# Kernel tuning notes

Hardware: AMD Instinct MI355X
Metric: run time of the kernel (lower is better)

## Reference

```python
import jax, jax.numpy as jnp
import numpy as np

NUM_EXPERTS = 8
TOP_K = 2
EMBED = 1024
FFN = 2048
GATE_HID = 1024


def setup_inputs() -> dict:
    key = jax.random.key(0)
    ks = jax.random.split(key, 8)
    s_e = 1.0 / np.sqrt(EMBED)
    s_f = 1.0 / np.sqrt(FFN)
    s_g = 1.0 / np.sqrt(GATE_HID)
    return {
        "hidden_states": jax.random.normal(ks[0], (2, 2048, EMBED), dtype=jnp.float32),
        # gate: Linear(EMBED->GATE_HID) with bias, ELU, Linear(GATE_HID->NUM_EXPERTS) with bias
        "gw1": jax.random.uniform(ks[1], (EMBED, GATE_HID), jnp.float32, -s_e, s_e),
        "gb1": jax.random.uniform(ks[2], (GATE_HID,), jnp.float32, -s_e, s_e),
        "gw2": jax.random.uniform(ks[3], (GATE_HID, NUM_EXPERTS), jnp.float32, -s_g, s_g),
        "gb2": jax.random.uniform(ks[4], (NUM_EXPERTS,), jnp.float32, -s_g, s_g),
        # experts (bias=False): w1,w3: EMBED->FFN ; w2: FFN->EMBED, stacked over experts
        "w1": jax.random.uniform(ks[5], (NUM_EXPERTS, EMBED, FFN), jnp.float32, -s_e, s_e),
        "w3": jax.random.uniform(ks[6], (NUM_EXPERTS, EMBED, FFN), jnp.float32, -s_e, s_e),
        "w2": jax.random.uniform(ks[7], (NUM_EXPERTS, FFN, EMBED), jnp.float32, -s_f, s_f),
    }


def reference(hidden_states, gw1, gb1, gw2, gb2, w1, w3, w2):
    B, S, H = hidden_states.shape
    x = hidden_states.reshape(-1, H)                      # [T, H]
    T = x.shape[0]
    # gate MLP
    g = jax.nn.elu(x @ gw1 + gb1)
    router_logits = g @ gw2 + gb2                         # [T, E]
    probs = jax.nn.softmax(router_logits.astype(jnp.float32), axis=-1)
    rw, sel = jax.lax.top_k(probs, TOP_K)                 # [T, K]
    rw = rw / jnp.sum(rw, axis=-1, keepdims=True)
    rw = rw.astype(hidden_states.dtype)
    # combine weights per (token, expert); full-capacity MoE == weighted sum
    combine = jnp.zeros((T, NUM_EXPERTS), dtype=hidden_states.dtype)
    combine = combine.at[jnp.arange(T)[:, None], sel].add(rw)   # [T, E]
    # expert MLPs computed densely then combined (math identical to gather/scatter)
    h = jax.nn.relu(jnp.einsum('th,ehf->etf', x, w1)) * jnp.einsum('th,ehf->etf', x, w3)
    y = jnp.einsum('etf,efh->eth', h, w2)                 # [E, T, H]
    out = jnp.einsum('eth,te->th', y, combine)            # [T, H]
    return out.reshape(B, S, H), router_logits
```

## Files before the change

kernel.cpp:

```cpp
#include <hip/hip_runtime.h>
#include <hip/hip_bf16.h>
#include <stdint.h>

#define TOKENS 4096
#define HDIM   1024
#define FDIM   2048
#define NEXP   8
#define NSLOTS (2 * TOKENS)
#define SLOTPAD (NSLOTS + 128)
#define RISKY_CAP 256
#define FLAG_THR 6e-3f

typedef __attribute__((ext_vector_type(4))) float        f32x4v;
typedef __attribute__((ext_vector_type(2))) float        f32x2v;
typedef __attribute__((ext_vector_type(4))) unsigned int u32x4v;
typedef __attribute__((ext_vector_type(8))) _Float16     f16x8v;

__device__ __forceinline__ unsigned short f2h(float f) {
  _Float16 h = (_Float16)f;
  union { _Float16 h; unsigned short u; } x; x.h = h; return x.u;
}

__device__ __forceinline__ void gload16(void* lds, const void* g) {
  __builtin_amdgcn_global_load_lds(
      reinterpret_cast<const __attribute__((address_space(1))) uint32_t*>(
          reinterpret_cast<uintptr_t>(g)),
      reinterpret_cast<__attribute__((address_space(3))) uint32_t*>(
          reinterpret_cast<uintptr_t>(lds)),
      16, 0, 0);
}

__global__ void k_convert_xh(const float* __restrict__ in, unsigned short* __restrict__ out) {
  const int i = (blockIdx.x * 256 + threadIdx.x) * 8;
  f32x4v a = *(const f32x4v*)(in + i);
  f32x4v b = *(const f32x4v*)(in + i + 4);
  u32x4v r;
  r[0] = (uint32_t)f2h(a[0]) | ((uint32_t)f2h(a[1]) << 16);
  r[1] = (uint32_t)f2h(a[2]) | ((uint32_t)f2h(a[3]) << 16);
  r[2] = (uint32_t)f2h(b[0]) | ((uint32_t)f2h(b[1]) << 16);
  r[3] = (uint32_t)f2h(b[2]) | ((uint32_t)f2h(b[3]) << 16);
  *(u32x4v*)(out + i) = r;
}

__device__ __forceinline__ void transpose_tile_v2(const float* __restrict__ ip,
                                                  unsigned short* __restrict__ op,
                                                  int R, int C, int r0, int c0) {
  __shared__ unsigned short tile[64][70];
  const int t = threadIdx.x;
  const int cp = (t & 15) * 4;
  const int rp = (t >> 4) * 2;
#pragma unroll
  for (int p = 0; p < 2; ++p) {
    const int r = rp + p * 32;
    f32x4v v0 = *(const f32x4v*)(ip + (size_t)(r0 + r) * C + c0 + cp);
    f32x4v v1 = *(const f32x4v*)(ip + (size_t)(r0 + r + 1) * C + c0 + cp);
#pragma unroll
    for (int j = 0; j < 4; ++j)
      *(uint32_t*)&tile[cp + j][r] = (uint32_t)f2h(v0[j]) | ((uint32_t)f2h(v1[j]) << 16);
  }
  __syncthreads();
  const int c = t >> 2, rc = (t & 3) * 16;
  uint32_t q[8];
#pragma unroll
  for (int j = 0; j < 8; ++j) q[j] = *(uint32_t*)&tile[c][rc + j * 2];
  unsigned short* o = op + (size_t)(c0 + c) * R + r0 + rc;
  u32x4v s0, s1;
  s0[0] = q[0]; s0[1] = q[1]; s0[2] = q[2]; s0[3] = q[3];
  s1[0] = q[4]; s1[1] = q[5]; s1[2] = q[6]; s1[3] = q[7];
  *(u32x4v*)o = s0;
  *(u32x4v*)(o + 8) = s1;
}

__global__ __launch_bounds__(256)
void k_transpose_v2(const float* __restrict__ in, unsigned short* __restrict__ out,
                    int R, int C) {
  const size_t mat = (size_t)R * C;
  transpose_tile_v2(in + (size_t)blockIdx.z * mat, out + (size_t)blockIdx.z * mat,
                    R, C, blockIdx.y * 64, blockIdx.x * 64);
}

__global__ __launch_bounds__(256)
void k_transpose_w13_v2(const float* __restrict__ w1, const float* __restrict__ w3,
                        unsigned short* __restrict__ o1, unsigned short* __restrict__ o3) {
  const int R = 1024, C = 2048;
  const size_t mat = (size_t)R * C;
  const int e = blockIdx.z & 7, which = blockIdx.z >> 3;
  const float* ip = (which ? w3 : w1) + (size_t)e * mat;
  unsigned short* op = (which ? o3 : o1) + (size_t)e * mat;
  transpose_tile_v2(ip, op, R, C, blockIdx.y * 64, blockIdx.x * 64);
}

__global__ __launch_bounds__(256)
void k_gate_f16(const unsigned short* __restrict__ Xh, const unsigned short* __restrict__ Bt,
                const float* __restrict__ gb1, float* __restrict__ G) {
  const int n0 = blockIdx.x * 64, m0 = blockIdx.y * 128;
  __shared__ unsigned short lA[128 * 64];
  __shared__ unsigned short lB[64 * 64];
  const int t = threadIdx.x, lane = t & 63, wv = t >> 6;

  const unsigned short *ap[4], *bp[2];
#pragma unroll
  for (int i = 0; i < 4; ++i) {
    const int gi = wv * 4 + i;
    const int row = gi * 8 + (lane >> 3);
    const int cs = (lane & 7) ^ (row & 7);
    ap[i] = Xh + (size_t)(m0 + row) * HDIM + cs * 8;
  }
#pragma unroll
  for (int i = 0; i < 2; ++i) {
    const int gi = wv * 2 + i;
    const int row = gi * 8 + (lane >> 3);
    const int cs = (lane & 7) ^ (row & 7);
    bp[i] = Bt + (size_t)(n0 + row) * HDIM + cs * 8;
  }

  f32x4v acc[4][2];
#pragma unroll
  for (int m = 0; m < 4; ++m)
#pragma unroll
    for (int n = 0; n < 2; ++n) acc[m][n] = (f32x4v){0.f, 0.f, 0.f, 0.f};

  const int wr = (wv >> 1) * 64, wc = (wv & 1) * 32;

  for (int k0 = 0; k0 < HDIM; k0 += 64) {
#pragma unroll
    for (int i = 0; i < 4; ++i) gload16(lA + (wv * 4 + i) * 512, ap[i] + k0);
#pragma unroll
    for (int i = 0; i < 2; ++i) gload16(lB + (wv * 2 + i) * 512, bp[i] + k0);
    __syncthreads();
#pragma unroll
    for (int kk = 0; kk < 2; ++kk) {
      const int ch = kk * 4 + (lane >> 4);
      f16x8v af[4];
#pragma unroll
      for (int m = 0; m < 4; ++m) {
        const int r = wr + m * 16 + (lane & 15);
        af[m] = *(const f16x8v*)(lA + r * 64 + (ch ^ (r & 7)) * 8);
      }
#pragma unroll
      for (int n = 0; n < 2; ++n) {
        const int r = wc + n * 16 + (lane & 15);
        f16x8v b = *(const f16x8v*)(lB + r * 64 + (ch ^ (r & 7)) * 8);
#pragma unroll
        for (int m = 0; m < 4; ++m)
          acc[m][n] = __builtin_amdgcn_mfma_f32_16x16x32_f16(af[m], b, acc[m][n], 0, 0, 0);
      }
    }
    __syncthreads();
  }
#pragma unroll
  for (int m = 0; m < 4; ++m)
#pragma unroll
    for (int n = 0; n < 2; ++n)
#pragma unroll
      for (int q = 0; q < 4; ++q) {
        const int row = m0 + wr + m * 16 + ((lane >> 4) << 2) + q;
        const int col = n0 + wc + n * 16 + (lane & 15);
        float x = acc[m][n][q] + gb1[col];
        G[(size_t)row * 1024 + col] = x > 0.f ? x : expm1f(x);
      }
}

__global__ void k_logits(const float* __restrict__ G, const float* __restrict__ gw2,
                         const float* __restrict__ gb2, float* __restrict__ Lg,
                         int* __restrict__ risky, int* __restrict__ rcnt) {
  const int lane = threadIdx.x & 63, wv = threadIdx.x >> 6;
  const int tok = blockIdx.x * 4 + wv;
  const float* g = G + (size_t)tok * 1024 + lane * 16;
  float acc[8];
#pragma unroll
  for (int j = 0; j < 8; ++j) acc[j] = 0.f;
#pragma unroll
  for (int c = 0; c < 16; c += 4) {
    f32x4v gv = *(const f32x4v*)(g + c);
#pragma unroll
    for (int u = 0; u < 4; ++u) {
      const float* wrow = gw2 + (size_t)(lane * 16 + c + u) * 8;
      f32x4v w0 = *(const f32x4v*)wrow;
      f32x4v w1 = *(const f32x4v*)(wrow + 4);
#pragma unroll
      for (int j = 0; j < 4; ++j) {
        acc[j]     += gv[u] * w0[j];
        acc[j + 4] += gv[u] * w1[j];
      }
    }
  }
#pragma unroll
  for (int s = 1; s < 64; s <<= 1)
#pragma unroll
    for (int j = 0; j < 8; ++j) acc[j] += __shfl_xor(acc[j], s, 64);
  if (lane == 0) {
    float l[8];
#pragma unroll
    for (int j = 0; j < 8; ++j) { l[j] = acc[j] + gb2[j]; Lg[(size_t)tok * 8 + j] = l[j]; }
    int i0 = 0; float v0 = l[0];
#pragma unroll
    for (int j = 1; j < 8; ++j) if (l[j] > v0) { v0 = l[j]; i0 = j; }
    int i1 = (i0 == 0) ? 1 : 0; float v1 = l[i1];
#pragma unroll
    for (int j = 0; j < 8; ++j) if (j != i0 && l[j] > v1) { v1 = l[j]; i1 = j; }
    float v2 = -1e30f;
#pragma unroll
    for (int j = 0; j < 8; ++j) if (j != i0 && j != i1 && l[j] > v2) v2 = l[j];
    if (v1 - v2 < FLAG_THR) {
      const int pos = atomicAdd(rcnt, 1);
      if (pos < RISKY_CAP) risky[pos] = tok;
    }
  }
}

__global__ __launch_bounds__(256)
void k_fixup_gs(const float* __restrict__ X, const float* __restrict__ gw1,
                const float* __restrict__ gb1, const int* __restrict__ risky,
                const int* __restrict__ rcnt, float* __restrict__ gsbuf) {
  __shared__ float xs[1024];
  __shared__ float red[128];
  int n = *rcnt; if (n > RISKY_CAP) n = RISKY_CAP;
  const int idx = blockIdx.y;
  if (idx >= n) return;
  const int tok = risky[idx];
  const int s0 = blockIdx.x * 128;
  const int t = threadIdx.x;
  for (int i = t; i < 1024; i += 256) xs[i] = X[(size_t)tok * 1024 + i];
  __syncthreads();
  const int h = t & 127, kh = t >> 7;
  const float* wp = gw1 + (size_t)(kh * 512) * 1024 + s0 + h;
  const float* xp = xs + kh * 512;
  float a0 = 0.f, a1 = 0.f, a2 = 0.f, a3 = 0.f;
  for (int k = 0; k < 512; k += 4) {
    a0 += xp[k]     * wp[(size_t)k * 1024];
    a1 += xp[k + 1] * wp[(size_t)(k + 1) * 1024];
    a2 += xp[k + 2] * wp[(size_t)(k + 2) * 1024];
    a3 += xp[k + 3] * wp[(size_t)(k + 3) * 1024];
  }
  const float acc = (a0 + a1) + (a2 + a3);
  if (kh == 1) red[h] = acc;
  __syncthreads();
  if (kh == 0) {
    const float v = acc + red[h] + gb1[s0 + h];
    gsbuf[(size_t)idx * 1024 + s0 + h] = v > 0.f ? v : expm1f(v);
  }
}

__global__ __launch_bounds__(256)
void k_fixup_lg(const float* __restrict__ gsbuf, const float* __restrict__ gw2,
                const float* __restrict__ gb2, const int* __restrict__ risky,
                const int* __restrict__ rcnt, float* __restrict__ Lg) {
  __shared__ float part[4][8];
  int n = *rcnt; if (n > RISKY_CAP) n = RISKY_CAP;
  const int idx = blockIdx.x;
  if (idx >= n) return;
  const int tok = risky[idx];
  const int t = threadIdx.x, lane = t & 63, wv = t >> 6;
  float lacc[8];
#pragma unroll
  for (int e = 0; e < 8; ++e) lacc[e] = 0.f;
#pragma unroll
  for (int j = 0; j < 4; ++j) {
    const int k = t * 4 + j;
    const float gv = gsbuf[(size_t)idx * 1024 + k];
    const float* w = gw2 + (size_t)k * 8;
#pragma unroll
    for (int e = 0; e < 8; ++e) lacc[e] += gv * w[e];
  }
#pragma unroll
  for (int s = 1; s < 64; s <<= 1)
#pragma unroll
    for (int e = 0; e < 8; ++e) lacc[e] += __shfl_xor(lacc[e], s, 64);
  if (lane == 0) {
#pragma unroll
    for (int e = 0; e < 8; ++e) part[wv][e] = lacc[e];
  }
  __syncthreads();
  if (t < 8) Lg[(size_t)tok * 8 + t] = part[0][t] + part[1][t] + part[2][t] + part[3][t] + gb2[t];
}

__global__ void k_top2(const float* __restrict__ Lg, int* __restrict__ tok_e,
                       float* __restrict__ tok_w, int* __restrict__ counts) {
  const int t = blockIdx.x * 256 + threadIdx.x;
  float l[8];
#pragma unroll
  for (int j = 0; j < 8; ++j) l[j] = Lg[(size_t)t * 8 + j];
  float mx = l[0];
#pragma unroll
  for (int j = 1; j < 8; ++j) mx = fmaxf(mx, l[j]);
  float p[8];
#pragma unroll
  for (int j = 0; j < 8; ++j) p[j] = expf(l[j] - mx);
  int i0 = 0; float b0 = p[0];
#pragma unroll
  for (int j = 1; j < 8; ++j) if (p[j] > b0) { b0 = p[j]; i0 = j; }
  int i1 = (i0 == 0) ? 1 : 0; float b1 = p[i1];
#pragma unroll
  for (int j = 0; j < 8; ++j) if (j != i0 && p[j] > b1) { b1 = p[j]; i1 = j; }
  const float inv = 1.f / (b0 + b1);
  tok_e[2 * t] = i0; tok_e[2 * t + 1] = i1;
  tok_w[2 * t] = b0 * inv; tok_w[2 * t + 1] = b1 * inv;
  atomicAdd(&counts[i0], 1);
  atomicAdd(&counts[i1], 1);
}

__global__ void k_offsets(const int* __restrict__ counts, int* __restrict__ offs,
                          int* __restrict__ curs) {
  if (threadIdx.x == 0) {
    int a = 0;
#pragma unroll
    for (int e = 0; e < NEXP; ++e) { offs[e] = a; a += counts[e]; }
  }
  if (threadIdx.x < NEXP) curs[threadIdx.x] = 0;
}

__global__ void k_assign(const int* __restrict__ tok_e, const float* __restrict__ tok_w,
                         const int* __restrict__ offs, int* __restrict__ curs,
                         int* __restrict__ slot_tok, float* __restrict__ slot_w,
                         int* __restrict__ tok2slot) {
  const int t = blockIdx.x * 256 + threadIdx.x;
#pragma unroll
  for (int k = 0; k < 2; ++k) {
    const int e = tok_e[2 * t + k];
    const int pos = atomicAdd(&curs[e], 1);
    const int slot = offs[e] + pos;
    slot_tok[slot] = t;
    slot_w[slot] = tok_w[2 * t + k];
    tok2slot[2 * t + k] = slot;
  }
}

__global__ __launch_bounds__(256, 2)
void k_gemm1(const unsigned short* __restrict__ Xh, const unsigned short* __restrict__ w1T,
             const unsigned short* __restrict__ w3T, const int* __restrict__ slot_tok,
             const int* __restrict__ counts, const int* __restrict__ offs,
             unsigned short* __restrict__ Hout) {
  const int e = blockIdx.z;
  const int cnt = counts[e];
  const int mt = blockIdx.y;
  if (mt * 128 >= cnt) return;
  const int base = offs[e] + mt * 128;
  const int n0 = blockIdx.x * 128;

  __shared__ unsigned short lA[128 * 64];
  __shared__ unsigned short lB1[128 * 64];
  __shared__ unsigned short lB3[128 * 64];
  __shared__ int tokid[128];

  const int t = threadIdx.x;
  if (t < 128) tokid[t] = slot_tok[base + t];
  __syncthreads();

  const int lane = t & 63, wv = t >> 6;
  const unsigned short *arow[4], *b1row[4], *b3row[4];
#pragma unroll
  for (int i = 0; i < 4; ++i) {
    const int gi = wv * 4 + i;
    const int row = gi * 8 + (lane >> 3);
    const int cs = (lane & 7) ^ (row & 7);
    arow[i] = Xh + (size_t)tokid[row] * HDIM + cs * 8;
    const int f = n0 + row;
    b1row[i] = w1T + ((size_t)e * FDIM + f) * HDIM + cs * 8;
    b3row[i] = w3T + ((size_t)e * FDIM + f) * HDIM + cs * 8;
  }

  f32x4v acc1[4][4], acc3[4][4];
#pragma unroll
  for (int m = 0; m < 4; ++m)
#pragma unroll
    for (int n = 0; n < 4; ++n) {
      acc1[m][n] = (f32x4v){0.f, 0.f, 0.f, 0.f};
      acc3[m][n] = (f32x4v){0.f, 0.f, 0.f, 0.f};
    }
  const int wr = (wv >> 1) * 64, wc = (wv & 1) * 64;

  for (int k0 = 0; k0 < HDIM; k0 += 64) {
#pragma unroll
    for (int i = 0; i < 4; ++i) {
      gload16(lA + (wv * 4 + i) * 512, arow[i] + k0);
      gload16(lB1 + (wv * 4 + i) * 512, b1row[i] + k0);
      gload16(lB3 + (wv * 4 + i) * 512, b3row[i] + k0);
    }
    __syncthreads();
#pragma unroll
    for (int kk = 0; kk < 64; kk += 32) {
      const int ch = (kk >> 3) + (lane >> 4);
      f16x8v af[4];
#pragma unroll
      for (int m = 0; m < 4; ++m) {
        const int r = wr + m * 16 + (lane & 15);
        af[m] = *(const f16x8v*)(lA + r * 64 + (ch ^ (r & 7)) * 8);
      }
#pragma unroll
      for (int n = 0; n < 4; ++n) {
        const int r = wc + n * 16 + (lane & 15);
        const int o = r * 64 + (ch ^ (r & 7)) * 8;
        f16x8v b1 = *(const f16x8v*)(lB1 + o);
        f16x8v b3 = *(const f16x8v*)(lB3 + o);
#pragma unroll
        for (int m = 0; m < 4; ++m) {
          acc1[m][n] = __builtin_amdgcn_mfma_f32_16x16x32_f16(af[m], b1, acc1[m][n], 0, 0, 0);
          acc3[m][n] = __builtin_amdgcn_mfma_f32_16x16x32_f16(af[m], b3, acc3[m][n], 0, 0, 0);
        }
      }
    }
    __syncthreads();
  }

  const int maxr = cnt - mt * 128;
#pragma unroll
  for (int m = 0; m < 4; ++m)
#pragma unroll
    for (int q = 0; q < 4; ++q) {
      const int rl = wr + m * 16 + ((lane >> 4) << 2) + q;
      if (rl < maxr) {
        unsigned short* hrow = Hout + (size_t)(base + rl) * FDIM;
#pragma unroll
        for (int n = 0; n < 4; ++n) {
          const int col = n0 + wc + n * 16 + (lane & 15);
          const float h = fmaxf(acc1[m][n][q], 0.f) * acc3[m][n][q];
          hrow[col] = f2h(h);
        }
      }
    }
}

__global__ __launch_bounds__(256, 2)
void k_gemm2(const unsigned short* __restrict__ Hin, const unsigned short* __restrict__ w2T,
             const int* __restrict__ counts, const int* __restrict__ offs,
             unsigned short* __restrict__ Y) {
  const int e = blockIdx.z;
  const int cnt = counts[e];
  const int mt = blockIdx.y;
  if (mt * 128 >= cnt) return;
  const int base = offs[e] + mt * 128;
  const int n0 = blockIdx.x * 128;

  __shared__ unsigned short lA[128 * 64];
  __shared__ unsigned short lB[128 * 64];

  const int t = threadIdx.x, lane = t & 63, wv = t >> 6;
  const unsigned short *arow[4], *brow[4];
#pragma unroll
  for (int i = 0; i < 4; ++i) {
    const int gi = wv * 4 + i;
    const int row = gi * 8 + (lane >> 3);
    const int cs = (lane & 7) ^ (row & 7);
    arow[i] = Hin + (size_t)(base + row) * FDIM + cs * 8;
    brow[i] = w2T + ((size_t)e * HDIM + n0 + row) * FDIM + cs * 8;
  }

  f32x4v acc[4][4];
#pragma unroll
  for (int m = 0; m < 4; ++m)
#pragma unroll
    for (int n = 0; n < 4; ++n) acc[m][n] = (f32x4v){0.f, 0.f, 0.f, 0.f};

  const int wr = (wv >> 1) * 64, wc = (wv & 1) * 64;

  for (int k0 = 0; k0 < FDIM; k0 += 64) {
#pragma unroll
    for (int i = 0; i < 4; ++i) {
      gload16(lA + (wv * 4 + i) * 512, arow[i] + k0);
      gload16(lB + (wv * 4 + i) * 512, brow[i] + k0);
    }
    __syncthreads();
#pragma unroll
    for (int kk = 0; kk < 64; kk += 32) {
      const int ch = (kk >> 3) + (lane >> 4);
      f16x8v af[4];
#pragma unroll
      for (int m = 0; m < 4; ++m) {
        const int r = wr + m * 16 + (lane & 15);
        af[m] = *(const f16x8v*)(lA + r * 64 + (ch ^ (r & 7)) * 8);
      }
#pragma unroll
      for (int n = 0; n < 4; ++n) {
        const int r = wc + n * 16 + (lane & 15);
        f16x8v b = *(const f16x8v*)(lB + r * 64 + (ch ^ (r & 7)) * 8);
#pragma unroll
        for (int m = 0; m < 4; ++m)
          acc[m][n] = __builtin_amdgcn_mfma_f32_16x16x32_f16(af[m], b, acc[m][n], 0, 0, 0);
      }
    }
    __syncthreads();
  }

  const int maxr = cnt - mt * 128;
#pragma unroll
  for (int m = 0; m < 4; ++m)
#pragma unroll
    for (int q = 0; q < 4; ++q) {
      const int rl = wr + m * 16 + ((lane >> 4) << 2) + q;
      if (rl < maxr) {
        unsigned short* yrow = Y + (size_t)(base + rl) * HDIM;
#pragma unroll
        for (int n = 0; n < 4; ++n) {
          const int col = n0 + wc + n * 16 + (lane & 15);
          yrow[col] = f2h(acc[m][n][q]);
        }
      }
    }
}

__global__ __launch_bounds__(256)
void k_combine(const unsigned short* __restrict__ Y, const int* __restrict__ tok2slot,
               const float* __restrict__ slot_w, float* __restrict__ out) {
  const int tok = blockIdx.x;
  const int s0 = tok2slot[2 * tok], s1 = tok2slot[2 * tok + 1];
  const float w0 = slot_w[s0], w1 = slot_w[s1];
  const int i = threadIdx.x * 4;
  const _Float16* y0 = (const _Float16*)(Y + (size_t)s0 * HDIM + i);
  const _Float16* y1 = (const _Float16*)(Y + (size_t)s1 * HDIM + i);
  f32x4v r;
#pragma unroll
  for (int j = 0; j < 4; ++j) r[j] = w0 * (float)y0[j] + w1 * (float)y1[j];
  *(f32x4v*)(out + (size_t)tok * HDIM + i) = r;
}

extern "C" void kernel_launch(void* const* d_in, const int* in_sizes, int n_in,
                              void* d_out, int out_size, void* d_ws, size_t ws_size,
                              hipStream_t stream) {
  const float* X   = (const float*)d_in[0];
  const float* gw1 = (const float*)d_in[1];
  const float* gb1 = (const float*)d_in[2];
  const float* gw2 = (const float*)d_in[3];
  const float* gb2 = (const float*)d_in[4];
  const float* w1  = (const float*)d_in[5];
  const float* w3  = (const float*)d_in[6];
  const float* w2  = (const float*)d_in[7];

  float* out = (float*)d_out;
  float* Lg  = out + (size_t)TOKENS * HDIM;

  char* ws = (char*)d_ws;
  size_t off = 0;
  auto alloc = [&](size_t b) { void* p = ws + off; off = (off + b + 255) & ~(size_t)255; return p; };

  unsigned short* Xh    = (unsigned short*)alloc((size_t)TOKENS * HDIM * 2);
  unsigned short* gw1T  = (unsigned short*)alloc((size_t)HDIM * 1024 * 2);
  unsigned short* w1T   = (unsigned short*)alloc((size_t)NEXP * FDIM * HDIM * 2);
  unsigned short* w3T   = (unsigned short*)alloc((size_t)NEXP * FDIM * HDIM * 2);
  unsigned short* w2T   = (unsigned short*)alloc((size_t)NEXP * HDIM * FDIM * 2);
  float*          G     = (float*)alloc((size_t)TOKENS * 1024 * 4);
  unsigned short* Hf    = (unsigned short*)alloc((size_t)SLOTPAD * FDIM * 2);
  unsigned short* Yb    = (unsigned short*)alloc((size_t)SLOTPAD * HDIM * 2);
  float*          gsbuf = (float*)alloc((size_t)RISKY_CAP * 1024 * 4);
  int*   tok_e    = (int*)alloc((size_t)TOKENS * 2 * 4);
  float* tok_w    = (float*)alloc((size_t)TOKENS * 2 * 4);
  int*   tok2slot = (int*)alloc((size_t)TOKENS * 2 * 4);
  int*   counts   = (int*)alloc(64);
  int*   offs     = (int*)alloc(64);
  int*   curs     = (int*)alloc(64);
  int*   slot_tok = (int*)alloc((size_t)SLOTPAD * 4);
  float* slot_w   = (float*)alloc((size_t)SLOTPAD * 4);
  int*   risky    = (int*)alloc((size_t)RISKY_CAP * 4);
  int*   rcnt     = (int*)alloc(64);

  hipMemsetAsync(counts, 0, 64, stream);
  hipMemsetAsync(rcnt, 0, 64, stream);
  hipMemsetAsync(slot_tok, 0, (size_t)SLOTPAD * 4, stream);

  k_convert_xh<<<dim3(TOKENS * HDIM / 2048), 256, 0, stream>>>(X, Xh);
  k_transpose_w13_v2<<<dim3(FDIM / 64, HDIM / 64, 2 * NEXP), 256, 0, stream>>>(w1, w3, w1T, w3T);
  k_transpose_v2<<<dim3(HDIM / 64, FDIM / 64, NEXP), 256, 0, stream>>>(w2, w2T, FDIM, HDIM);
  k_transpose_v2<<<dim3(16, 16, 1), 256, 0, stream>>>(gw1, gw1T, 1024, 1024);
  k_gate_f16<<<dim3(1024 / 64, TOKENS / 128), 256, 0, stream>>>(Xh, gw1T, gb1, G);
  k_logits<<<dim3(TOKENS / 4), 256, 0, stream>>>(G, gw2, gb2, Lg, risky, rcnt);
  k_fixup_gs<<<dim3(8, RISKY_CAP), 256, 0, stream>>>(X, gw1, gb1, risky, rcnt, gsbuf);
  k_fixup_lg<<<dim3(RISKY_CAP), 256, 0, stream>>>(gsbuf, gw2, gb2, risky, rcnt, Lg);
  k_top2<<<dim3(TOKENS / 256), 256, 0, stream>>>(Lg, tok_e, tok_w, counts);
  k_offsets<<<dim3(1), 64, 0, stream>>>(counts, offs, curs);
  k_assign<<<dim3(TOKENS / 256), 256, 0, stream>>>(tok_e, tok_w, offs, curs, slot_tok, slot_w, tok2slot);
  k_gemm1<<<dim3(FDIM / 128, TOKENS / 128, NEXP), 256, 0, stream>>>(Xh, w1T, w3T, slot_tok, counts, offs, Hf);
  k_gemm2<<<dim3(HDIM / 128, TOKENS / 128, NEXP), 256, 0, stream>>>(Hf, w2T, counts, offs, Yb);
  k_combine<<<dim3(TOKENS), 256, 0, stream>>>(Yb, tok2slot, slot_w, out);
}
```

Baseline: 373.5 us.

## Fuse gate GEMM, X conversion and weight transposes into one launch

Merges the X fp16 conversion, the w1/w3/w2 transposes and the gate GEMM into a single kernel that dispatches on block index, so the independent prep work can overlap with the gate GEMM. The gate GEMM now converts X from fp32 to fp16 on the fly instead of waiting for Xh. The gate hidden activations are stored as fp16 instead of fp32, which halves that traffic but adds rounding before the logits, which the risky-token fixup path must absorb. SLOTPAD is also enlarged.

```diff
diff --git a/kernel.cpp b/kernel.cpp
--- a/kernel.cpp
+++ b/kernel.cpp
@@ -7,12 +7,11 @@
 #define FDIM   2048
 #define NEXP   8
 #define NSLOTS (2 * TOKENS)
-#define SLOTPAD (NSLOTS + 128)
+#define SLOTPAD (NSLOTS + 256)
 #define RISKY_CAP 256
 #define FLAG_THR 6e-3f
 
 typedef __attribute__((ext_vector_type(4))) float        f32x4v;
-typedef __attribute__((ext_vector_type(2))) float        f32x2v;
 typedef __attribute__((ext_vector_type(4))) unsigned int u32x4v;
 typedef __attribute__((ext_vector_type(8))) _Float16     f16x8v;
 
@@ -30,18 +29,6 @@
       16, 0, 0);
 }
 
-__global__ void k_convert_xh(const float* __restrict__ in, unsigned short* __restrict__ out) {
-  const int i = (blockIdx.x * 256 + threadIdx.x) * 8;
-  f32x4v a = *(const f32x4v*)(in + i);
-  f32x4v b = *(const f32x4v*)(in + i + 4);
-  u32x4v r;
-  r[0] = (uint32_t)f2h(a[0]) | ((uint32_t)f2h(a[1]) << 16);
-  r[1] = (uint32_t)f2h(a[2]) | ((uint32_t)f2h(a[3]) << 16);
-  r[2] = (uint32_t)f2h(b[0]) | ((uint32_t)f2h(b[1]) << 16);
-  r[3] = (uint32_t)f2h(b[2]) | ((uint32_t)f2h(b[3]) << 16);
-  *(u32x4v*)(out + i) = r;
-}
-
 __device__ __forceinline__ void transpose_tile_v2(const float* __restrict__ ip,
                                                   unsigned short* __restrict__ op,
                                                   int R, int C, int r0, int c0) {
@@ -72,117 +59,152 @@
 }
 
 __global__ __launch_bounds__(256)
-void k_transpose_v2(const float* __restrict__ in, unsigned short* __restrict__ out,
-                    int R, int C) {
-  const size_t mat = (size_t)R * C;
-  transpose_tile_v2(in + (size_t)blockIdx.z * mat, out + (size_t)blockIdx.z * mat,
-                    R, C, blockIdx.y * 64, blockIdx.x * 64);
-}
-
+void k_prep0(const float* __restrict__ gw1, unsigned short* __restrict__ og1) {
+  transpose_tile_v2(gw1, og1, 1024, 1024, (blockIdx.x >> 4) * 64, (blockIdx.x & 15) * 64);
+}
+
+#define NB_GATE 512
+#define NB_CONV 2048
+#define NB_W13  8192
+#define NB_W2   4096
 __global__ __launch_bounds__(256)
-void k_transpose_w13_v2(const float* __restrict__ w1, const float* __restrict__ w3,
-                        unsigned short* __restrict__ o1, unsigned short* __restrict__ o3) {
-  const int R = 1024, C = 2048;
-  const size_t mat = (size_t)R * C;
-  const int e = blockIdx.z & 7, which = blockIdx.z >> 3;
-  const float* ip = (which ? w3 : w1) + (size_t)e * mat;
-  unsigned short* op = (which ? o3 : o1) + (size_t)e * mat;
-  transpose_tile_v2(ip, op, R, C, blockIdx.y * 64, blockIdx.x * 64);
-}
-
-__global__ __launch_bounds__(256)
-void k_gate_f16(const unsigned short* __restrict__ Xh, const unsigned short* __restrict__ Bt,
-                const float* __restrict__ gb1, float* __restrict__ G) {
-  const int n0 = blockIdx.x * 64, m0 = blockIdx.y * 128;
-  __shared__ unsigned short lA[128 * 64];
-  __shared__ unsigned short lB[64 * 64];
-  const int t = threadIdx.x, lane = t & 63, wv = t >> 6;
-
-  const unsigned short *ap[4], *bp[2];
-#pragma unroll
-  for (int i = 0; i < 4; ++i) {
-    const int gi = wv * 4 + i;
-    const int row = gi * 8 + (lane >> 3);
-    const int cs = (lane & 7) ^ (row & 7);
-    ap[i] = Xh + (size_t)(m0 + row) * HDIM + cs * 8;
-  }
-#pragma unroll
-  for (int i = 0; i < 2; ++i) {
-    const int gi = wv * 2 + i;
-    const int row = gi * 8 + (lane >> 3);
-    const int cs = (lane & 7) ^ (row & 7);
-    bp[i] = Bt + (size_t)(n0 + row) * HDIM + cs * 8;
-  }
-
-  f32x4v acc[4][2];
-#pragma unroll
-  for (int m = 0; m < 4; ++m)
-#pragma unroll
-    for (int n = 0; n < 2; ++n) acc[m][n] = (f32x4v){0.f, 0.f, 0.f, 0.f};
-
-  const int wr = (wv >> 1) * 64, wc = (wv & 1) * 32;
-
-  for (int k0 = 0; k0 < HDIM; k0 += 64) {
-#pragma unroll
-    for (int i = 0; i < 4; ++i) gload16(lA + (wv * 4 + i) * 512, ap[i] + k0);
-#pragma unroll
-    for (int i = 0; i < 2; ++i) gload16(lB + (wv * 2 + i) * 512, bp[i] + k0);
-    __syncthreads();
-#pragma unroll
-    for (int kk = 0; kk < 2; ++kk) {
-      const int ch = kk * 4 + (lane >> 4);
-      f16x8v af[4];
-#pragma unroll
-      for (int m = 0; m < 4; ++m) {
-        const int r = wr + m * 16 + (lane & 15);
-        af[m] = *(const f16x8v*)(lA + r * 64 + (ch ^ (r & 7)) * 8);
-      }
-#pragma unroll
-      for (int n = 0; n < 2; ++n) {
-        const int r = wc + n * 16 + (lane & 15);
-        f16x8v b = *(const f16x8v*)(lB + r * 64 + (ch ^ (r & 7)) * 8);
-#pragma unroll
-        for (int m = 0; m < 4; ++m)
-          acc[m][n] = __builtin_amdgcn_mfma_f32_16x16x32_f16(af[m], b, acc[m][n], 0, 0, 0);
-      }
-    }
-    __syncthreads();
-  }
-#pragma unroll
-  for (int m = 0; m < 4; ++m)
-#pragma unroll
-    for (int n = 0; n < 2; ++n)
-#pragma unroll
-      for (int q = 0; q < 4; ++q) {
-        const int row = m0 + wr + m * 16 + ((lane >> 4) << 2) + q;
-        const int col = n0 + wc + n * 16 + (lane & 15);
-        float x = acc[m][n][q] + gb1[col];
-        G[(size_t)row * 1024 + col] = x > 0.f ? x : expm1f(x);
-      }
-}
-
-__global__ void k_logits(const float* __restrict__ G, const float* __restrict__ gw2,
+void k_fused(const float* __restrict__ X, unsigned short* __restrict__ Xh,
+             const float* __restrict__ w1, const float* __restrict__ w3,
+             unsigned short* __restrict__ o1, unsigned short* __restrict__ o3,
+             const float* __restrict__ w2, unsigned short* __restrict__ o2,
+             const unsigned short* __restrict__ gw1T, const float* __restrict__ gb1,
+             unsigned short* __restrict__ Gh) {
+  const int id = blockIdx.x;
+  const int t = threadIdx.x;
+  if (id < NB_GATE) {
+    __shared__ unsigned short lA[128 * 64];
+    __shared__ unsigned short lB[64 * 64];
+    const int n0 = (id & 15) * 64, m0 = (id >> 4) * 128;
+    const int lane = t & 63, wv = t >> 6;
+
+    const unsigned short* bp[2];
+#pragma unroll
+    for (int i = 0; i < 2; ++i) {
+      const int gi = wv * 2 + i;
+      const int row = gi * 8 + (lane >> 3);
+      const int cs = (lane & 7) ^ (row & 7);
+      bp[i] = gw1T + (size_t)(n0 + row) * HDIM + cs * 8;
+    }
+
+    f32x4v acc[4][2];
+#pragma unroll
+    for (int m = 0; m < 4; ++m)
+#pragma unroll
+      for (int n = 0; n < 2; ++n) acc[m][n] = (f32x4v){0.f, 0.f, 0.f, 0.f};
+
+    const int wr = (wv >> 1) * 64, wc = (wv & 1) * 32;
+
+    for (int k0 = 0; k0 < HDIM; k0 += 64) {
+#pragma unroll
+      for (int p = 0; p < 4; ++p) {
+        const int ga = p * 256 + t;
+        const int r = ga >> 3, c = ga & 7;
+        const float* s = X + (size_t)(m0 + r) * HDIM + k0 + c * 8;
+        f32x4v v0 = *(const f32x4v*)s;
+        f32x4v v1 = *(const f32x4v*)(s + 4);
+        u32x4v pk;
+        pk[0] = (uint32_t)f2h(v0[0]) | ((uint32_t)f2h(v0[1]) << 16);
+        pk[1] = (uint32_t)f2h(v0[2]) | ((uint32_t)f2h(v0[3]) << 16);
+        pk[2] = (uint32_t)f2h(v1[0]) | ((uint32_t)f2h(v1[1]) << 16);
+        pk[3] = (uint32_t)f2h(v1[2]) | ((uint32_t)f2h(v1[3]) << 16);
+        *(u32x4v*)&lA[r * 64 + ((c ^ (r & 7)) * 8)] = pk;
+      }
+#pragma unroll
+      for (int i = 0; i < 2; ++i) gload16(lB + (wv * 2 + i) * 512, bp[i] + k0);
+      __syncthreads();
+#pragma unroll
+      for (int kk = 0; kk < 2; ++kk) {
+        const int ch = kk * 4 + (lane >> 4);
+        f16x8v af[4];
+#pragma unroll
+        for (int m = 0; m < 4; ++m) {
+          const int r = wr + m * 16 + (lane & 15);
+          af[m] = *(const f16x8v*)(lA + r * 64 + (ch ^ (r & 7)) * 8);
+        }
+#pragma unroll
+        for (int n = 0; n < 2; ++n) {
+          const int r = wc + n * 16 + (lane & 15);
+          f16x8v b = *(const f16x8v*)(lB + r * 64 + (ch ^ (r & 7)) * 8);
+#pragma unroll
+          for (int m = 0; m < 4; ++m)
+            acc[m][n] = __builtin_amdgcn_mfma_f32_16x16x32_f16(af[m], b, acc[m][n], 0, 0, 0);
+        }
+      }
+      __syncthreads();
+    }
+#pragma unroll
+    for (int m = 0; m < 4; ++m)
+#pragma unroll
+      for (int n = 0; n < 2; ++n)
+#pragma unroll
+        for (int q = 0; q < 4; ++q) {
+          const int row = m0 + wr + m * 16 + ((lane >> 4) << 2) + q;
+          const int col = n0 + wc + n * 16 + (lane & 15);
+          float x = acc[m][n][q] + gb1[col];
+          Gh[(size_t)row * 1024 + col] = f2h(x > 0.f ? x : expm1f(x));
+        }
+    return;
+  }
+  int b = id - NB_GATE;
+  if (b < NB_CONV) {
+    const int i = (b * 256 + t) * 8;
+    f32x4v a = *(const f32x4v*)(X + i);
+    f32x4v c = *(const f32x4v*)(X + i + 4);
+    u32x4v r;
+    r[0] = (uint32_t)f2h(a[0]) | ((uint32_t)f2h(a[1]) << 16);
+    r[1] = (uint32_t)f2h(a[2]) | ((uint32_t)f2h(a[3]) << 16);
+    r[2] = (uint32_t)f2h(c[0]) | ((uint32_t)f2h(c[1]) << 16);
+    r[3] = (uint32_t)f2h(c[2]) | ((uint32_t)f2h(c[3]) << 16);
+    *(u32x4v*)(Xh + i) = r;
+    return;
+  }
+  b -= NB_CONV;
+  if (b < NB_W13) {
+    const int bx = b & 31, by = (b >> 5) & 15, bz = b >> 9;
+    const int e = bz & 7, which = bz >> 3;
+    const size_t mat = (size_t)1024 * 2048;
+    transpose_tile_v2((which ? w3 : w1) + (size_t)e * mat,
+                      (which ? o3 : o1) + (size_t)e * mat,
+                      1024, 2048, by * 64, bx * 64);
+    return;
+  }
+  b -= NB_W13;
+  {
+    const int bx = b & 15, by = (b >> 4) & 31, e = b >> 9;
+    const size_t mat = (size_t)2048 * 1024;
+    transpose_tile_v2(w2 + (size_t)e * mat, o2 + (size_t)e * mat,
+                      2048, 1024, by * 64, bx * 64);
+  }
+}
+
+__global__ void k_logits(const unsigned short* __restrict__ Gh, const float* __restrict__ gw2,
                          const float* __restrict__ gb2, float* __restrict__ Lg,
                          int* __restrict__ risky, int* __restrict__ rcnt) {
   const int lane = threadIdx.x & 63, wv = threadIdx.x >> 6;
   const int tok = blockIdx.x * 4 + wv;
-  const float* g = G + (size_t)tok * 1024 + lane * 16;
+  const unsigned short* g = Gh + (size_t)tok * 1024 + lane * 16;
+  f16x8v g0 = *(const f16x8v*)g;
+  f16x8v g1 = *(const f16x8v*)(g + 8);
+  float gv[16];
+#pragma unroll
+  for (int j = 0; j < 8; ++j) { gv[j] = (float)g0[j]; gv[8 + j] = (float)g1[j]; }
   float acc[8];
 #pragma unroll
   for (int j = 0; j < 8; ++j) acc[j] = 0.f;
 #pragma unroll
-  for (int c = 0; c < 16; c += 4) {
-    f32x4v gv = *(const f32x4v*)(g + c);
-#pragma unroll
-    for (int u = 0; u < 4; ++u) {
-      const float* wrow = gw2 + (size_t)(lane * 16 + c + u) * 8;
-      f32x4v w0 = *(const f32x4v*)wrow;
-      f32x4v w1 = *(const f32x4v*)(wrow + 4);
-#pragma unroll
-      for (int j = 0; j < 4; ++j) {
-        acc[j]     += gv[u] * w0[j];
-        acc[j + 4] += gv[u] * w1[j];
-      }
+  for (int u = 0; u < 16; ++u) {
+    const float* wrow = gw2 + (size_t)(lane * 16 + u) * 8;
+    f32x4v w0 = *(const f32x4v*)wrow;
+    f32x4v w1 = *(const f32x4v*)(wrow + 4);
+#pragma unroll
+    for (int j = 0; j < 4; ++j) {
+      acc[j]     += gv[u] * w0[j];
+      acc[j + 4] += gv[u] * w1[j];
     }
   }
 #pragma unroll
@@ -538,7 +560,7 @@
   unsigned short* w1T   = (unsigned short*)alloc((size_t)NEXP * FDIM * HDIM * 2);
   unsigned short* w3T   = (unsigned short*)alloc((size_t)NEXP * FDIM * HDIM * 2);
   unsigned short* w2T   = (unsigned short*)alloc((size_t)NEXP * HDIM * FDIM * 2);
-  float*          G     = (float*)alloc((size_t)TOKENS * 1024 * 4);
+  unsigned short* Gh    = (unsigned short*)alloc((size_t)TOKENS * 1024 * 2);
   unsigned short* Hf    = (unsigned short*)alloc((size_t)SLOTPAD * FDIM * 2);
   unsigned short* Yb    = (unsigned short*)alloc((size_t)SLOTPAD * HDIM * 2);
   float*          gsbuf = (float*)alloc((size_t)RISKY_CAP * 1024 * 4);
@@ -557,12 +579,10 @@
   hipMemsetAsync(rcnt, 0, 64, stream);
   hipMemsetAsync(slot_tok, 0, (size_t)SLOTPAD * 4, stream);
 
-  k_convert_xh<<<dim3(TOKENS * HDIM / 2048), 256, 0, stream>>>(X, Xh);
-  k_transpose_w13_v2<<<dim3(FDIM / 64, HDIM / 64, 2 * NEXP), 256, 0, stream>>>(w1, w3, w1T, w3T);
-  k_transpose_v2<<<dim3(HDIM / 64, FDIM / 64, NEXP), 256, 0, stream>>>(w2, w2T, FDIM, HDIM);
-  k_transpose_v2<<<dim3(16, 16, 1), 256, 0, stream>>>(gw1, gw1T, 1024, 1024);
-  k_gate_f16<<<dim3(1024 / 64, TOKENS / 128), 256, 0, stream>>>(Xh, gw1T, gb1, G);
-  k_logits<<<dim3(TOKENS / 4), 256, 0, stream>>>(G, gw2, gb2, Lg, risky, rcnt);
+  k_prep0<<<dim3(256), 256, 0, stream>>>(gw1, gw1T);
+  k_fused<<<dim3(NB_GATE + NB_CONV + NB_W13 + NB_W2), 256, 0, stream>>>(
+      X, Xh, w1, w3, w1T, w3T, w2, w2T, gw1T, gb1, Gh);
+  k_logits<<<dim3(TOKENS / 4), 256, 0, stream>>>(Gh, gw2, gb2, Lg, risky, rcnt);
   k_fixup_gs<<<dim3(8, RISKY_CAP), 256, 0, stream>>>(X, gw1, gb1, risky, rcnt, gsbuf);
   k_fixup_lg<<<dim3(RISKY_CAP), 256, 0, stream>>>(gsbuf, gw2, gb2, risky, rcnt, Lg);
   k_top2<<<dim3(TOKENS / 256), 256, 0, stream>>>(Lg, tok_e, tok_w, counts);
```

Result: no change. 369.7 us (-1.0%).
